# Performance work log

Measured on AMD Instinct MI355X. Metric: run time of the kernel, lower is better.

## Reference

```python
import jax, jax.numpy as jnp
import numpy as np

C = 1.0          # curvature parameter (constraint <x,x>_L = -1/C)
EPS = 1e-7
N_NODES = 50000
D = 128
N_EDGES = 800000


def _l_inner(u, v):
    # Lorentz (Minkowski) inner product: -u0*v0 + <u_s, v_s>
    return -u[..., 0] * v[..., 0] + jnp.sum(u[..., 1:] * v[..., 1:], axis=-1)


def _proj(x, c=C):
    # recompute time coordinate so x lies on the hyperboloid
    sp = x[:, 1:]
    x0 = jnp.sqrt(1.0 / c + jnp.sum(sp * sp, axis=-1, keepdims=True))
    return jnp.concatenate([x0, sp], axis=-1)


def _logmap0(x, c=C):
    sqc = jnp.sqrt(c)
    x0, sp = x[:, :1], x[:, 1:]
    y = jnp.clip(sqc * x0, 1.0 + EPS, None)
    d = jnp.arccosh(y) / sqc                                   # geodesic distance to origin
    sn = jnp.clip(jnp.linalg.norm(sp, axis=-1, keepdims=True), EPS, None)
    return jnp.concatenate([jnp.zeros_like(x0), d * sp / sn], axis=-1)


def _expmap0(u, c=C):
    sqc = jnp.sqrt(c)
    sp = u[:, 1:]
    un = jnp.clip(jnp.linalg.norm(sp, axis=-1, keepdims=True), EPS, None)
    th = sqc * un
    x0 = jnp.cosh(th) / sqc
    return jnp.concatenate([x0, jnp.sinh(th) * sp / th], axis=-1)


def setup_inputs() -> dict:
    key = jax.random.key(0)
    k1, k2, k3 = jax.random.split(key, 3)
    x_raw = jax.random.normal(k1, (N_NODES, D), dtype=jnp.float32) * 0.5
    x = _proj(x_raw)  # valid points on the Lorentz manifold
    # xavier-uniform-like scale for (127,127) weight
    lim = float(np.sqrt(6.0 / (2 * (D - 1))))
    weight = jax.random.uniform(k2, (D - 1, D - 1), dtype=jnp.float32, minval=-lim, maxval=lim)
    bias = jnp.zeros((D - 1,), dtype=jnp.float32)
    edge_index = jax.random.randint(k3, (2, N_EDGES), 0, N_NODES, dtype=jnp.int64)
    return {"x": x, "weight": weight, "bias": bias, "edge_index": edge_index}


def reference(x, weight, bias, edge_index):
    c = C
    # ---- HyperbolicLinear (lorentz): log0 -> spatial matmul + bias -> exp0 -> proj
    v = _logmap0(x, c)                         # [N, D], time comp = 0
    out_space = v[:, 1:] @ weight.T + bias     # [N, D-1]
    out = jnp.concatenate([v[:, :1], out_space], axis=-1)
    h = _proj(_expmap0(out, c), c)             # [N, D] on manifold
    # ---- HyperbolicDistAtt: gather -> lorentz distance -> exp(-d)
    row, col = edge_index[0], edge_index[1]
    xi = h[row]                                # [E, D]
    xj = h[col]                                # [E, D]
    inner = _l_inner(xi, xj)                   # [E]
    dist = jnp.arccosh(jnp.clip(-c * inner, 1.0 + EPS, None)) / jnp.sqrt(c)
    att = jnp.exp(-dist)                       # [E]
    # ---- Lorentz centroid: weighted sum then Minkowski-norm normalization
    num = jax.ops.segment_sum(att[:, None] * xj, row, num_segments=h.shape[0])  # [N, D]
    denom = jnp.sqrt(c) * jnp.sqrt(jnp.clip(-_l_inner(num, num), EPS, None))    # [N]
    return num / denom[:, None]
```

## Files before the change

### kernel.cpp

```cpp
#include <hip/hip_runtime.h>
#include <math.h>

#define EPS 1e-7f
#define CAP 64
#define REC_INTS   34
#define REC_USH    68
#define LIST_OFF    4

typedef __attribute__((ext_vector_type(8))) short short8;
typedef __attribute__((ext_vector_type(4))) float floatx4;

__device__ inline short f2bf(float f) {
    union { float f; unsigned u; } v; v.f = f;
    unsigned r = v.u + 0x7FFF + ((v.u >> 16) & 1);
    return (short)(r >> 16);
}

__device__ inline float fast_sqrt(float x) { return __builtin_amdgcn_sqrtf(x); }
__device__ inline float fast_rcp(float x)  { return __builtin_amdgcn_rcpf(x); }
__device__ inline float fast_rsq(float x)  { return __builtin_amdgcn_rsqf(x); }

__global__ __launch_bounds__(256) void prep_w(
    const float* __restrict__ weight, short* __restrict__ wfg,
    int* __restrict__ rec, int N)
{
    int idx = blockIdx.x * 256 + threadIdx.x;
    if (idx < 128 * 128) {
        int j = idx >> 7, k = idx & 127;
        float w = (j < 127 && k >= 1) ? weight[j * 127 + (k - 1)] : 0.0f;
        int tt = j >> 4, cc = j & 15, ss = k >> 5, qq = (k >> 3) & 3, ee = k & 7;
        wfg[(((tt * 4 + ss) * 64) + qq * 16 + cc) * 8 + ee] = f2bf(w);
    }
    if (rec) {
        for (int r = idx; r < N; r += gridDim.x * 256) rec[(size_t)r * REC_INTS] = 0;
    }
}

__global__ __launch_bounds__(256) void transform_mfma(
    const float* __restrict__ x, const short* __restrict__ wfg,
    const float* __restrict__ bias, float* __restrict__ h, int N)
{
    __shared__ __align__(16) short Wf[8 * 4 * 64 * 8];
    __shared__ __align__(16) short Vf[4 * 4 * 64 * 8];

    const int t = threadIdx.x;
    const int lane = t & 63;
    const int wv = t >> 6;
    const int c = lane & 15;
    const int q = lane >> 4;

    {
        const short8* src = (const short8*)wfg;
        short8* dst = (short8*)Wf;
        #pragma unroll
        for (int it = 0; it < 8; ++it) dst[it * 256 + t] = src[it * 256 + t];
    }
    float bvals[8];
    #pragma unroll
    for (int tt = 0; tt < 8; ++tt) {
        int j = tt * 16 + c;
        bvals[tt] = (j < 127) ? bias[j] : 0.0f;
    }
    __syncthreads();

    const short8* wfp = (const short8*)Wf;
    const short8* vfp = (const short8*)Vf + wv * 256;
    short8* vw = (short8*)Vf;

    const int nchunks = (N + 63) >> 6;
    for (int chunk = blockIdx.x; chunk < nchunks; chunk += gridDim.x) {
        const int base = chunk * 64;

        {
            int nl = t >> 2;
            int qt = t & 3;
            int n = base + nl;
            const float4* xr = (const float4*)(x + (size_t)n * 128 + qt * 32);
            float4 xv[8];
            if (n < N) {
                #pragma unroll
                for (int g = 0; g < 8; ++g) xv[g] = xr[g];
            } else {
                #pragma unroll
                for (int g = 0; g < 8; ++g) xv[g] = make_float4(0, 0, 0, 0);
            }
            float ss = 0.0f;
            #pragma unroll
            for (int g = 0; g < 8; ++g)
                ss += xv[g].x * xv[g].x + xv[g].y * xv[g].y +
                      xv[g].z * xv[g].z + xv[g].w * xv[g].w;
            float x0 = xv[0].x;
            if (qt == 0) ss -= x0 * x0;
            ss += __shfl_xor(ss, 1, 64);
            ss += __shfl_xor(ss, 2, 64);
            x0 = __shfl(x0, lane & ~3, 64);
            float sn = fmaxf(fast_sqrt(ss), EPS);
            float xc = fmaxf(x0, 1.0f + EPS);
            float dd = __logf(xc + fast_sqrt(xc * xc - 1.0f));
            float coef = dd * fast_rcp(sn);
            int wreg = nl >> 4, cn = nl & 15;
            #pragma unroll
            for (int g = 0; g < 4; ++g) {
                float4 a = xv[2 * g], b = xv[2 * g + 1];
                short8 pk;
                pk[0] = f2bf(coef * a.x); pk[1] = f2bf(coef * a.y);
                pk[2] = f2bf(coef * a.z); pk[3] = f2bf(coef * a.w);
                pk[4] = f2bf(coef * b.x); pk[5] = f2bf(coef * b.y);
                pk[6] = f2bf(coef * b.z); pk[7] = f2bf(coef * b.w);
                vw[wreg * 256 + qt * 64 + g * 16 + cn] = pk;
            }
        }

        floatx4 acc[8];
        #pragma unroll
        for (int tt = 0; tt < 8; ++tt) acc[tt] = (floatx4){0, 0, 0, 0};
        #pragma unroll
        for (int s = 0; s < 4; ++s) {
            short8 af = vfp[s * 64 + lane];
            #pragma unroll
            for (int tt = 0; tt < 8; ++tt) {
                short8 bf = wfp[(tt * 4 + s) * 64 + lane];
                acc[tt] = __builtin_amdgcn_mfma_f32_16x16x32_bf16(af, bf, acc[tt], 0, 0, 0);
            }
        }

        float rs[4] = {0, 0, 0, 0};
        #pragma unroll
        for (int tt = 0; tt < 8; ++tt) {
            #pragma unroll
            for (int r = 0; r < 4; ++r) {
                float v = acc[tt][r] + bvals[tt];
                acc[tt][r] = v;
                rs[r] += v * v;
            }
        }
        #pragma unroll
        for (int r = 0; r < 4; ++r) {
            rs[r] += __shfl_xor(rs[r], 1, 64);
            rs[r] += __shfl_xor(rs[r], 2, 64);
            rs[r] += __shfl_xor(rs[r], 4, 64);
            rs[r] += __shfl_xor(rs[r], 8, 64);
        }
        int nodebase = base + wv * 16 + q * 4;
        #pragma unroll
        for (int r = 0; r < 4; ++r) {
            int n = nodebase + r;
            if (n < N) {
                float th = fmaxf(fast_sqrt(rs[r]), EPS);
                float ex = __expf(th);
                float sc_big = (ex - fast_rcp(ex)) * 0.5f * fast_rcp(th);
                float sc_small = 1.0f + th * th * (1.0f / 6.0f);
                float scale = (th < 1e-3f) ? sc_small : sc_big;
                float* hr = h + (size_t)n * 128;
                #pragma unroll
                for (int tt = 0; tt < 8; ++tt) {
                    int j = tt * 16 + c;
                    if (j < 127) hr[1 + j] = scale * acc[tt][r];
                    else         hr[0] = fast_sqrt(1.0f + scale * scale * rs[r]);
                }
            }
        }
    }
}

__global__ __launch_bounds__(256) void scatter_cap(
    const int* __restrict__ rows, const int* __restrict__ cols,
    int* __restrict__ rec, int E)
{
    int i = blockIdx.x * 256 + threadIdx.x;
    if (i < E) {
        int r = rows[i];
        int p = atomicAdd(rec + (size_t)r * REC_INTS, 1);
        if (p < CAP)
            ((ushort*)rec)[(size_t)r * REC_USH + LIST_OFF + p] = (ushort)cols[i];
    }
}

__global__ __launch_bounds__(256) void agg_cap(
    const float* __restrict__ h, const int* __restrict__ rec,
    float* __restrict__ out, int N)
{
    int wid = (int)((blockIdx.x * 256u + threadIdx.x) >> 6);
    int nw = (int)(gridDim.x * 4u);
    int lane = threadIdx.x & 63;
    int q = lane >> 4;
    int i = lane & 15;

    for (int n = wid; n < N; n += nw) {
        int deg = rec[(size_t)n * REC_INTS];
        if (deg > CAP) deg = CAP;
        const ushort* lst = (const ushort*)rec + (size_t)n * REC_USH + LIST_OFF;
        int ec = (lane < deg) ? (int)lst[lane] : 0;

        const float4* hn = (const float4*)(h + (size_t)n * 128) + 2 * i;
        float4 xa = hn[0], xb = hn[1];
        float xa0 = (i == 0) ? -xa.x : xa.x;
        float acc[8] = {0, 0, 0, 0, 0, 0, 0, 0};

        for (int kb = 0; kb < deg; kb += 16) {
            int k0 = kb + q;
            bool v0 = k0      < deg;
            bool v1 = k0 + 4  < deg;
            bool v2 = k0 + 8  < deg;
            bool v3 = k0 + 12 < deg;
            int c0 = __shfl(ec, k0,      64);
            int c1 = __shfl(ec, k0 + 4,  64);
            int c2 = __shfl(ec, k0 + 8,  64);
            int c3 = __shfl(ec, k0 + 12, 64);
            float4 a0 = {0,0,0,0}, b0 = {0,0,0,0};
            float4 a1 = {0,0,0,0}, b1 = {0,0,0,0};
            float4 a2 = {0,0,0,0}, b2 = {0,0,0,0};
            float4 a3 = {0,0,0,0}, b3 = {0,0,0,0};
            if (v0) { const float4* p = (const float4*)(h + (size_t)c0 * 128) + 2 * i; a0 = p[0]; b0 = p[1]; }
            if (v1) { const float4* p = (const float4*)(h + (size_t)c1 * 128) + 2 * i; a1 = p[0]; b1 = p[1]; }
            if (v2) { const float4* p = (const float4*)(h + (size_t)c2 * 128) + 2 * i; a2 = p[0]; b2 = p[1]; }
            if (v3) { const float4* p = (const float4*)(h + (size_t)c3 * 128) + 2 * i; a3 = p[0]; b3 = p[1]; }

            float s0 = xa0 * a0.x + xa.y * a0.y + xa.z * a0.z + xa.w * a0.w
                     + xb.x * b0.x + xb.y * b0.y + xb.z * b0.z + xb.w * b0.w;
            float s1 = xa0 * a1.x + xa.y * a1.y + xa.z * a1.z + xa.w * a1.w
                     + xb.x * b1.x + xb.y * b1.y + xb.z * b1.z + xb.w * b1.w;
            float s2 = xa0 * a2.x + xa.y * a2.y + xa.z * a2.z + xa.w * a2.w
                     + xb.x * b2.x + xb.y * b2.y + xb.z * b2.z + xb.w * b2.w;
            float s3 = xa0 * a3.x + xa.y * a3.y + xa.z * a3.z + xa.w * a3.w
                     + xb.x * b3.x + xb.y * b3.y + xb.z * b3.z + xb.w * b3.w;
            #pragma unroll
            for (int o = 1; o <= 8; o <<= 1) {
                s0 += __shfl_xor(s0, o, 64);
                s1 += __shfl_xor(s1, o, 64);
                s2 += __shfl_xor(s2, o, 64);
                s3 += __shfl_xor(s3, o, 64);
            }
            float z0 = fmaxf(-s0, 1.0f + EPS);
            float z1 = fmaxf(-s1, 1.0f + EPS);
            float z2 = fmaxf(-s2, 1.0f + EPS);
            float z3 = fmaxf(-s3, 1.0f + EPS);
            float att0 = v0 ? fast_rcp(z0 + fast_sqrt(z0 * z0 - 1.0f)) : 0.0f;
            float att1 = v1 ? fast_rcp(z1 + fast_sqrt(z1 * z1 - 1.0f)) : 0.0f;
            float att2 = v2 ? fast_rcp(z2 + fast_sqrt(z2 * z2 - 1.0f)) : 0.0f;
            float att3 = v3 ? fast_rcp(z3 + fast_sqrt(z3 * z3 - 1.0f)) : 0.0f;
            acc[0] += att0 * a0.x + att1 * a1.x + att2 * a2.x + att3 * a3.x;
            acc[1] += att0 * a0.y + att1 * a1.y + att2 * a2.y + att3 * a3.y;
            acc[2] += att0 * a0.z + att1 * a1.z + att2 * a2.z + att3 * a3.z;
            acc[3] += att0 * a0.w + att1 * a1.w + att2 * a2.w + att3 * a3.w;
            acc[4] += att0 * b0.x + att1 * b1.x + att2 * b2.x + att3 * b3.x;
            acc[5] += att0 * b0.y + att1 * b1.y + att2 * b2.y + att3 * b3.y;
            acc[6] += att0 * b0.z + att1 * b1.z + att2 * b2.z + att3 * b3.z;
            acc[7] += att0 * b0.w + att1 * b1.w + att2 * b2.w + att3 * b3.w;
        }

        #pragma unroll
        for (int k = 0; k < 8; ++k) {
            acc[k] += __shfl_xor(acc[k], 16, 64);
            acc[k] += __shfl_xor(acc[k], 32, 64);
        }

        float part = 0.0f;
        #pragma unroll
        for (int k = 0; k < 8; ++k) part -= acc[k] * acc[k];
        if (i == 0) part += 2.0f * acc[0] * acc[0];
        #pragma unroll
        for (int o = 1; o <= 8; o <<= 1) part += __shfl_xor(part, o, 64);
        float inv = fast_rsq(fmaxf(part, EPS));

        if (q == 0) {
            float4* op = (float4*)(out + (size_t)n * 128) + 2 * i;
            op[0] = make_float4(acc[0] * inv, acc[1] * inv, acc[2] * inv, acc[3] * inv);
            op[1] = make_float4(acc[4] * inv, acc[5] * inv, acc[6] * inv, acc[7] * inv);
        }
    }
}

__global__ __launch_bounds__(256) void hist_kernel(
    const int* __restrict__ rows, int* __restrict__ deg, int E)
{
    int i = blockIdx.x * 256 + threadIdx.x;
    if (i < E) atomicAdd(&deg[rows[i]], 1);
}

__global__ __launch_bounds__(1024) void scan1(
    const int* __restrict__ deg, int* __restrict__ off,
    int* __restrict__ bsum, int N)
{
    __shared__ int wsum[16];
    __shared__ int wexcl[16];
    int i = blockIdx.x * 1024 + threadIdx.x;
    int lane = threadIdx.x & 63, wid = threadIdx.x >> 6;
    int v = (i < N) ? deg[i] : 0;
    int incl = v;
    #pragma unroll
    for (int o = 1; o < 64; o <<= 1) {
        int u = __shfl_up(incl, o, 64);
        if (lane >= o) incl += u;
    }
    if (lane == 63) wsum[wid] = incl;
    __syncthreads();
    if (wid == 0 && lane < 16) {
        int s = wsum[lane];
        int si = s;
        #pragma unroll
        for (int o = 1; o < 16; o <<= 1) {
            int u = __shfl_up(si, o, 64);
            if (lane >= o) si += u;
        }
        wexcl[lane] = si - s;
        if (lane == 15) bsum[blockIdx.x] = si;
    }
    __syncthreads();
    if (i < N) off[i] = wexcl[wid] + incl - v;
}

__global__ __launch_bounds__(64) void scan2(int* __restrict__ bsum, int nb)
{
    int lane = threadIdx.x & 63;
    int v = (lane < nb) ? bsum[lane] : 0;
    int si = v;
    #pragma unroll
    for (int o = 1; o < 64; o <<= 1) {
        int u = __shfl_up(si, o, 64);
        if (lane >= o) si += u;
    }
    if (lane < nb) bsum[lane] = si - v;
}

__global__ __launch_bounds__(1024) void scan3(
    int* __restrict__ off, int* __restrict__ pos,
    const int* __restrict__ bsum, int N, int E)
{
    int i = blockIdx.x * 1024 + threadIdx.x;
    if (i < N) {
        int v = off[i] + bsum[blockIdx.x];
        off[i] = v;
        pos[i] = v;
    }
    if (i == 0) off[N] = E;
}

__global__ __launch_bounds__(256) void scatter_kernel(
    const int* __restrict__ rows, const int* __restrict__ cols,
    int* __restrict__ pos, int* __restrict__ ecol, int E)
{
    int i = blockIdx.x * 256 + threadIdx.x;
    if (i < E) {
        int p = atomicAdd(&pos[rows[i]], 1);
        ecol[p] = cols[i];
    }
}

__global__ __launch_bounds__(256) void agg_kernel(
    const float* __restrict__ h, const int* __restrict__ off,
    const int* __restrict__ ecol, float* __restrict__ out, int N)
{
    int wid = (int)((blockIdx.x * 256u + threadIdx.x) >> 6);
    int nw = (int)(gridDim.x * 4u);
    int lane = threadIdx.x & 63;
    int q = lane >> 4;
    int i = lane & 15;

    for (int n = wid; n < N; n += nw) {
        const float4* hn = (const float4*)(h + (size_t)n * 128) + 2 * i;
        float4 xa = hn[0], xb = hn[1];
        float xa0 = (i == 0) ? -xa.x : xa.x;
        float acc[8] = {0, 0, 0, 0, 0, 0, 0, 0};
        int e0 = off[n], e1 = off[n + 1];

        int e = e0 + q;
        for (; e + 4 < e1; e += 8) {
            int c0 = ecol[e];
            int c1 = ecol[e + 4];
            const float4* p0 = (const float4*)(h + (size_t)c0 * 128) + 2 * i;
            const float4* p1 = (const float4*)(h + (size_t)c1 * 128) + 2 * i;
            float4 a0 = p0[0], b0 = p0[1];
            float4 a1 = p1[0], b1 = p1[1];
            float s0 = xa0 * a0.x + xa.y * a0.y + xa.z * a0.z + xa.w * a0.w
                     + xb.x * b0.x + xb.y * b0.y + xb.z * b0.z + xb.w * b0.w;
            float s1 = xa0 * a1.x + xa.y * a1.y + xa.z * a1.z + xa.w * a1.w
                     + xb.x * b1.x + xb.y * b1.y + xb.z * b1.z + xb.w * b1.w;
            #pragma unroll
            for (int o = 1; o <= 8; o <<= 1) {
                s0 += __shfl_xor(s0, o, 64);
                s1 += __shfl_xor(s1, o, 64);
            }
            float z0 = fmaxf(-s0, 1.0f + EPS);
            float z1 = fmaxf(-s1, 1.0f + EPS);
            float att0 = fast_rcp(z0 + fast_sqrt(z0 * z0 - 1.0f));
            float att1 = fast_rcp(z1 + fast_sqrt(z1 * z1 - 1.0f));
            acc[0] += att0 * a0.x + att1 * a1.x;
            acc[1] += att0 * a0.y + att1 * a1.y;
            acc[2] += att0 * a0.z + att1 * a1.z;
            acc[3] += att0 * a0.w + att1 * a1.w;
            acc[4] += att0 * b0.x + att1 * b1.x;
            acc[5] += att0 * b0.y + att1 * b1.y;
            acc[6] += att0 * b0.z + att1 * b1.z;
            acc[7] += att0 * b0.w + att1 * b1.w;
        }
        if (e < e1) {
            int c0 = ecol[e];
            const float4* p0 = (const float4*)(h + (size_t)c0 * 128) + 2 * i;
            float4 a0 = p0[0], b0 = p0[1];
            float s0 = xa0 * a0.x + xa.y * a0.y + xa.z * a0.z + xa.w * a0.w
                     + xb.x * b0.x + xb.y * b0.y + xb.z * b0.z + xb.w * b0.w;
            #pragma unroll
            for (int o = 1; o <= 8; o <<= 1) s0 += __shfl_xor(s0, o, 64);
            float z0 = fmaxf(-s0, 1.0f + EPS);
            float att0 = fast_rcp(z0 + fast_sqrt(z0 * z0 - 1.0f));
            acc[0] += att0 * a0.x;
            acc[1] += att0 * a0.y;
            acc[2] += att0 * a0.z;
            acc[3] += att0 * a0.w;
            acc[4] += att0 * b0.x;
            acc[5] += att0 * b0.y;
            acc[6] += att0 * b0.z;
            acc[7] += att0 * b0.w;
        }

        #pragma unroll
        for (int k = 0; k < 8; ++k) {
            acc[k] += __shfl_xor(acc[k], 16, 64);
            acc[k] += __shfl_xor(acc[k], 32, 64);
        }

        float part = 0.0f;
        #pragma unroll
        for (int k = 0; k < 8; ++k) part -= acc[k] * acc[k];
        if (i == 0) part += 2.0f * acc[0] * acc[0];
        #pragma unroll
        for (int o = 1; o <= 8; o <<= 1) part += __shfl_xor(part, o, 64);
        float inv = fast_rsq(fmaxf(part, EPS));

        if (q == 0) {
            float4* op = (float4*)(out + (size_t)n * 128) + 2 * i;
            op[0] = make_float4(acc[0] * inv, acc[1] * inv, acc[2] * inv, acc[3] * inv);
            op[1] = make_float4(acc[4] * inv, acc[5] * inv, acc[6] * inv, acc[7] * inv);
        }
    }
}

__global__ __launch_bounds__(256) void edge_kernel(
    const float* __restrict__ h, const int* __restrict__ rows,
    const int* __restrict__ cols, float* __restrict__ num, int E)
{
    int wid = (int)((blockIdx.x * 256u + threadIdx.x) >> 6);
    if (wid >= E) return;
    int lane = threadIdx.x & 63;
    int r = rows[wid];
    int c = cols[wid];
    const float2* h2 = (const float2*)h;
    float2 xi = h2[(size_t)r * 64 + lane];
    float2 xj = h2[(size_t)c * 64 + lane];
    float p = (lane == 0 ? -xi.x * xj.x : xi.x * xj.x) + xi.y * xj.y;
    #pragma unroll
    for (int off = 32; off >= 1; off >>= 1) p += __shfl_xor(p, off, 64);
    float z = fmaxf(-p, 1.0f + EPS);
    float att = fast_rcp(z + fast_sqrt(z * z - 1.0f));
    float* dst = num + (size_t)r * 128 + 2 * lane;
    atomicAdd(dst, att * xj.x);
    atomicAdd(dst + 1, att * xj.y);
}

__global__ __launch_bounds__(256) void norm_kernel(float* __restrict__ num, int N)
{
    int wid = (int)((blockIdx.x * 256u + threadIdx.x) >> 6);
    int nw = (int)((gridDim.x * 256u) >> 6);
    int lane = threadIdx.x & 63;
    for (int n = wid; n < N; n += nw) {
        float2* p2 = (float2*)(num + (size_t)n * 128);
        float2 v = p2[lane];
        float q = (lane == 0) ? (v.x * v.x - v.y * v.y) : (-v.x * v.x - v.y * v.y);
        #pragma unroll
        for (int o = 32; o >= 1; o >>= 1) q += __shfl_xor(q, o, 64);
        float inv = fast_rsq(fmaxf(q, EPS));
        p2[lane] = make_float2(v.x * inv, v.y * inv);
    }
}

extern "C" void kernel_launch(void* const* d_in, const int* in_sizes, int n_in,
                              void* d_out, int out_size, void* d_ws, size_t ws_size,
                              hipStream_t stream)
{
    const float* x      = (const float*)d_in[0];
    const float* weight = (const float*)d_in[1];
    const float* bias   = (const float*)d_in[2];
    const int*   edge   = (const int*)d_in[3];

    const int N = in_sizes[0] / 128;
    const int E = in_sizes[3] / 2;
    const int* rows = edge;
    const int* cols = edge + E;

    char* base = (char*)d_ws;
    float* h   = (float*)base;                       base += (size_t)N * 128 * 4;
    short* wfg = (short*)base;                       base += (size_t)128 * 128 * 2;
    char* rest = base;
    size_t head = (size_t)(rest - (char*)d_ws);

    int* rec = (int*)rest;
    size_t need_cap = head + (size_t)N * REC_INTS * 4;

    int* deg  = (int*)rest;
    int* off  = deg + N;
    int* pos  = off + (N + 1);
    int* bsum = pos + N;
    int* ecol = bsum + 64;
    size_t need_csr = head + ((size_t)N * 3 + 65 + E) * 4;

    const int nchunks = (N + 63) >> 6;

    if (ws_size >= need_cap && N <= 65535) {
        prep_w<<<64, 256, 0, stream>>>(weight, wfg, rec, N);
        transform_mfma<<<nchunks, 256, 0, stream>>>(x, wfg, bias, h, N);
        scatter_cap<<<(E + 255) / 256, 256, 0, stream>>>(rows, cols, rec, E);
        agg_cap<<<(N + 3) / 4, 256, 0, stream>>>(h, rec, (float*)d_out, N);
    } else if (ws_size >= need_csr) {
        prep_w<<<64, 256, 0, stream>>>(weight, wfg, deg, N);
        transform_mfma<<<nchunks, 256, 0, stream>>>(x, wfg, bias, h, N);
        const int nsb = (N + 1023) / 1024;
        hist_kernel<<<(E + 255) / 256, 256, 0, stream>>>(rows, deg, E);
        scan1<<<nsb, 1024, 0, stream>>>(deg, off, bsum, N);
        scan2<<<1, 64, 0, stream>>>(bsum, nsb);
        scan3<<<nsb, 1024, 0, stream>>>(off, pos, bsum, N, E);
        scatter_kernel<<<(E + 255) / 256, 256, 0, stream>>>(rows, cols, pos, ecol, E);
        agg_kernel<<<(N + 3) / 4, 256, 0, stream>>>(h, off, ecol, (float*)d_out, N);
    } else {
        prep_w<<<64, 256, 0, stream>>>(weight, wfg, (int*)nullptr, 0);
        transform_mfma<<<nchunks, 256, 0, stream>>>(x, wfg, bias, h, N);
        hipMemsetAsync(d_out, 0, (size_t)out_size * sizeof(float), stream);
        edge_kernel<<<(E + 3) / 4, 256, 0, stream>>>(h, rows, cols, (float*)d_out, E);
        norm_kernel<<<2048, 256, 0, stream>>>((float*)d_out, N);
    }
}
```

Measured before the change: 189.2 us.

## Read weights from global, batch scatter atomics, and widen prep_w grid

The transform kernel no longer stages the bf16 weight fragments in LDS and reads them straight from global memory. This removes the LDS copy and block barrier, but every MFMA operand load now goes to cache. The scatter kernel has each thread handle four edges, using nontemporal loads and grouped atomics to expose more memory-level parallelism. agg_cap now loads the neighbour list without waiting on the degree, and prep_w runs with more blocks so the record clearing finishes faster.

```diff
diff --git a/kernel.cpp b/kernel.cpp
--- a/kernel.cpp
+++ b/kernel.cpp
@@ -40,7 +40,6 @@
     const float* __restrict__ x, const short* __restrict__ wfg,
     const float* __restrict__ bias, float* __restrict__ h, int N)
 {
-    __shared__ __align__(16) short Wf[8 * 4 * 64 * 8];
     __shared__ __align__(16) short Vf[4 * 4 * 64 * 8];
 
     const int t = threadIdx.x;
@@ -49,21 +48,14 @@
     const int c = lane & 15;
     const int q = lane >> 4;
 
-    {
-        const short8* src = (const short8*)wfg;
-        short8* dst = (short8*)Wf;
-        #pragma unroll
-        for (int it = 0; it < 8; ++it) dst[it * 256 + t] = src[it * 256 + t];
-    }
     float bvals[8];
     #pragma unroll
     for (int tt = 0; tt < 8; ++tt) {
         int j = tt * 16 + c;
         bvals[tt] = (j < 127) ? bias[j] : 0.0f;
     }
-    __syncthreads();
-
-    const short8* wfp = (const short8*)Wf;
+
+    const short8* wfp = (const short8*)wfg;
     const short8* vfp = (const short8*)Vf + wv * 256;
     short8* vw = (short8*)Vf;
 
@@ -167,13 +159,26 @@
     const int* __restrict__ rows, const int* __restrict__ cols,
     int* __restrict__ rec, int E)
 {
-    int i = blockIdx.x * 256 + threadIdx.x;
-    if (i < E) {
-        int r = rows[i];
-        int p = atomicAdd(rec + (size_t)r * REC_INTS, 1);
-        if (p < CAP)
-            ((ushort*)rec)[(size_t)r * REC_USH + LIST_OFF + p] = (ushort)cols[i];
-    }
+    int base = blockIdx.x * 1024 + (int)threadIdx.x;
+    int r[4], c[4], p[4];
+    bool val[4];
+    #pragma unroll
+    for (int e = 0; e < 4; ++e) {
+        int i = base + 256 * e;
+        val[e] = i < E;
+        r[e] = 0; c[e] = 0;
+        if (val[e]) {
+            r[e] = __builtin_nontemporal_load(rows + i);
+            c[e] = __builtin_nontemporal_load(cols + i);
+        }
+    }
+    #pragma unroll
+    for (int e = 0; e < 4; ++e)
+        if (val[e]) p[e] = atomicAdd(rec + (size_t)r[e] * REC_INTS, 1);
+    #pragma unroll
+    for (int e = 0; e < 4; ++e)
+        if (val[e] && p[e] < CAP)
+            ((ushort*)rec)[(size_t)r[e] * REC_USH + LIST_OFF + p[e]] = (ushort)c[e];
 }
 
 __global__ __launch_bounds__(256) void agg_cap(
@@ -187,10 +192,10 @@
     int i = lane & 15;
 
     for (int n = wid; n < N; n += nw) {
+        const ushort* lst = (const ushort*)rec + (size_t)n * REC_USH + LIST_OFF;
+        int ec = (int)lst[lane];
         int deg = rec[(size_t)n * REC_INTS];
         if (deg > CAP) deg = CAP;
-        const ushort* lst = (const ushort*)rec + (size_t)n * REC_USH + LIST_OFF;
-        int ec = (lane < deg) ? (int)lst[lane] : 0;
 
         const float4* hn = (const float4*)(h + (size_t)n * 128) + 2 * i;
         float4 xa = hn[0], xb = hn[1];
@@ -507,12 +512,12 @@
     const int nchunks = (N + 63) >> 6;
 
     if (ws_size >= need_cap && N <= 65535) {
-        prep_w<<<64, 256, 0, stream>>>(weight, wfg, rec, N);
+        prep_w<<<256, 256, 0, stream>>>(weight, wfg, rec, N);
         transform_mfma<<<nchunks, 256, 0, stream>>>(x, wfg, bias, h, N);
-        scatter_cap<<<(E + 255) / 256, 256, 0, stream>>>(rows, cols, rec, E);
+        scatter_cap<<<(E + 1023) / 1024, 256, 0, stream>>>(rows, cols, rec, E);
         agg_cap<<<(N + 3) / 4, 256, 0, stream>>>(h, rec, (float*)d_out, N);
     } else if (ws_size >= need_csr) {
-        prep_w<<<64, 256, 0, stream>>>(weight, wfg, deg, N);
+        prep_w<<<256, 256, 0, stream>>>(weight, wfg, deg, N);
         transform_mfma<<<nchunks, 256, 0, stream>>>(x, wfg, bias, h, N);
         const int nsb = (N + 1023) / 1024;
         hist_kernel<<<(E + 255) / 256, 256, 0, stream>>>(rows, deg, E);
@@ -522,7 +527,7 @@
         scatter_kernel<<<(E + 255) / 256, 256, 0, stream>>>(rows, cols, pos, ecol, E);
         agg_kernel<<<(N + 3) / 4, 256, 0, stream>>>(h, off, ecol, (float*)d_out, N);
     } else {
-        prep_w<<<64, 256, 0, stream>>>(weight, wfg, (int*)nullptr, 0);
+        prep_w<<<256, 256, 0, stream>>>(weight, wfg, (int*)nullptr, 0);
         transform_mfma<<<nchunks, 256, 0, stream>>>(x, wfg, bias, h, N);
         hipMemsetAsync(d_out, 0, (size_t)out_size * sizeof(float), stream);
         edge_kernel<<<(E + 3) / 4, 256, 0, stream>>>(h, rows, cols, (float*)d_out, E);
```

Result: no change. 191.9 us (+1.4%).
